# Kernel tuning notes

Hardware: AMD Instinct MI355X
Metric: run time of the kernel (lower is better)

## Reference

```python
import jax, jax.numpy as jnp
import numpy as np

B, N, C = 64, 197, 768
H = 12
D = C // H
SCALE = D ** -0.5
TAU = 5.0
THRESHOLD = 0.6
NEG_INF = float('-inf')


def setup_inputs() -> dict:
    key = jax.random.key(0)
    ks = jax.random.split(key, 10)
    def gumbel(k, shape):
        # -log(Exponential) == standard Gumbel noise, matches torch exponential_().log()
        e = jax.random.exponential(k, shape, dtype=jnp.float32)
        return -jnp.log(e + 1e-10)
    s = 0.02
    return {
        'x': jax.random.normal(ks[0], (B, N, C), dtype=jnp.float32),
        'g1': gumbel(ks[1], (B, N - 1, 1)),
        'g2': gumbel(ks[2], (B, N - 1, 1)),
        'Wq': jax.random.normal(ks[3], (C, C), dtype=jnp.float32) * s,
        'Wk': jax.random.normal(ks[4], (C, C), dtype=jnp.float32) * s,
        'Wv': jax.random.normal(ks[5], (C, C), dtype=jnp.float32) * s,
        'Wp': jax.random.normal(ks[6], (C, C), dtype=jnp.float32) * s,
        'bp': jnp.zeros((C,), dtype=jnp.float32),
        'Wm': jax.random.normal(ks[7], (1, C), dtype=jnp.float32) * s,
        'bm': jnp.zeros((1,), dtype=jnp.float32),
    }


def reference(x, g1, g2, Wq, Wk, Wv, Wp, bp, Wm, bm):
    b, n, c = x.shape
    # QKV projections (qkv_bias=False), reshape to (B, H, N, D)
    q = (x @ Wq.T).reshape(b, n, H, D).transpose(0, 2, 1, 3)
    k = (x @ Wk.T).reshape(b, n, H, D).transpose(0, 2, 1, 3)
    v = (x @ Wv.T).reshape(b, n, H, D).transpose(0, 2, 1, 3)

    attn_pre = jnp.einsum('bhnd,bhmd->bhnm', q, k) * SCALE  # (B,H,N,N)

    # SimpleTokenSelect: gumbel-sigmoid gating on non-CLS tokens (training=True, hard=True)
    logits = x[:, 1:] @ Wm.T + bm                       # (B, N-1, 1)
    y_soft = jax.nn.sigmoid((logits + g1 - g2) / TAU)
    y_hard = (y_soft > THRESHOLD).astype(y_soft.dtype)
    ts = y_hard - jax.lax.stop_gradient(y_soft) + y_soft  # straight-through
    ts = jnp.concatenate([jnp.ones((b, 1, 1), dtype=ts.dtype), ts], axis=1)[..., 0]  # (B, N)

    # attention policy = outer product of token gates, detached (ada_token_detach_attn)
    policy = jax.lax.stop_gradient(jnp.einsum('bn,bm->bnm', ts, ts))[:, None]  # (B,1,N,N)

    # pre-softmax masking: zero gated scores, -inf off-diagonal entries of gated rows
    eye = jnp.eye(n, dtype=attn_pre.dtype)
    neg_mask = jnp.where(1.0 - policy - eye > 0, NEG_INF, 0.0)
    attn = jax.nn.softmax(attn_pre * policy + neg_mask, axis=-1)

    out = jnp.einsum('bhnm,bhmd->bhnd', attn, v)        # (B,H,N,D)
    out = out.transpose(0, 2, 1, 3).reshape(b, n, c)
    out = out @ Wp.T + bp                                # proj (dropout p=0)
    return out
```

## Files before the change

### kernel.cpp

```cpp
#include <hip/hip_runtime.h>
#include <hip/hip_bf16.h>
#include <cstdint>

typedef unsigned short u16;
typedef __attribute__((ext_vector_type(8))) short bf16x8;
typedef __attribute__((ext_vector_type(4))) float f32x4;

#define NB 64
#define NN 197
#define NC 768
#define NH 12
#define ND 64
#define NM (NB*NN)
#define CAP 96
#define ASZ ((size_t)NM*NC)
#define WSZ ((size_t)NC*NC)
#define SELSZ ((size_t)NB*CAP*NC)

__device__ __forceinline__ u16 f2bf(float f) {
  uint32_t u = __float_as_uint(f);
  u += 0x7fffu + ((u >> 16) & 1u);
  return (u16)(u >> 16);
}

__device__ __forceinline__ void gl_lds16(const u16* g, u16* l) {
  __builtin_amdgcn_global_load_lds(
      (const __attribute__((address_space(1))) void*)g,
      (__attribute__((address_space(3))) void*)l, 16, 0, 0);
}

__device__ __forceinline__ int self_compact(const float* __restrict__ ts, int b,
                                            int* sidx, unsigned long long* bmask) {
  int t = threadIdx.x, lane = t & 63, wave = t >> 6;
  bool sel = (t < NN) && (ts[b * NN + t] > 0.5f);
  unsigned long long m = __ballot(sel);
  if (lane == 0) bmask[wave] = m;
  for (int i = t; i < CAP; i += 256) sidx[i] = 0;
  __syncthreads();
  int before = 0, total = 0;
  #pragma unroll
  for (int w = 0; w < 4; ++w) {
    int c = __popcll(bmask[w]);
    total += c;
    if (w < wave) before += c;
  }
  int within = __popcll(bmask[wave] & ((lane == 0) ? 0ull : (~0ull >> (64 - lane))));
  int pos = before + within;
  int cntc = total < CAP ? total : CAP;
  if (sel && pos < CAP) sidx[pos] = t;
  __syncthreads();
  return cntc;
}

#define GATEB 3152
#define XBLK 9456
#define WBLK 576
#define TRBLK 144
__global__ __launch_bounds__(256) void k1_prep(const float* __restrict__ x,
    const float* __restrict__ g1, const float* __restrict__ g2,
    const float* __restrict__ Wm, const float* __restrict__ bm,
    const float* __restrict__ wq, const float* __restrict__ wk,
    const float* __restrict__ wv, const float* __restrict__ wp,
    u16* __restrict__ xb, u16* __restrict__ wqb, u16* __restrict__ wkb,
    u16* __restrict__ wvb, u16* __restrict__ wpb, u16* __restrict__ wvt,
    float* __restrict__ ts) {
  __shared__ u16 T[64][72];
  int bid = blockIdx.x, tid = threadIdx.x;

  if (bid < GATEB) {
    int wave = tid >> 6, lane = tid & 63;
    int wid = bid * 4 + wave;
    int b = wid / NN, n = wid % NN;
    float o = 1.0f;
    if (n != 0) {
      const float* xr = x + (size_t)wid * NC;
      double acc = 0.0;
      #pragma unroll
      for (int i = 0; i < 12; ++i)
        acc += (double)xr[lane + 64*i] * (double)Wm[lane + 64*i];
      #pragma unroll
      for (int off = 32; off; off >>= 1) acc += __shfl_down(acc, off);
      double z = (acc + (double)bm[0] + (double)g1[b*(NN-1) + n - 1]
                                      - (double)g2[b*(NN-1) + n - 1]) / 5.0;
      o = (z > 0.4054651081081643820) ? 1.0f : 0.0f;
      o = __shfl(o, 0);
    }
    if (lane == 0) ts[wid] = o;
    return;
  }
  bid -= GATEB;
  if (bid < XBLK) {
    int i = bid * 256 + tid;
    float4 f = ((const float4*)x)[i];
    ushort4 o;
    o.x = f2bf(f.x); o.y = f2bf(f.y); o.z = f2bf(f.z); o.w = f2bf(f.w);
    ((ushort4*)xb)[i] = o;
    return;
  }
  bid -= XBLK;
  if (bid < 4*WBLK) {
    int seg = bid / WBLK;
    int i = (bid - seg * WBLK) * 256 + tid;
    const float* src; u16* dst;
    if (seg == 0)      { src = wq; dst = wqb; }
    else if (seg == 1) { src = wk; dst = wkb; }
    else if (seg == 2) { src = wv; dst = wvb; }
    else               { src = wp; dst = wpb; }
    float4 f = ((const float4*)src)[i];
    ushort4 o;
    o.x = f2bf(f.x); o.y = f2bf(f.y); o.z = f2bf(f.z); o.w = f2bf(f.w);
    ((ushort4*)dst)[i] = o;
    return;
  }
  bid -= 4*WBLK;
  {
    int bx = bid % 12, by = bid / 12;
    int j0 = by * 64, k0 = bx * 64;
    #pragma unroll
    for (int g = 0; g < 4; ++g) {
      int r = g * 16 + (tid >> 4);
      int c4 = (tid & 15) * 4;
      float4 f = *(const float4*)(wv + (size_t)(j0 + r) * NC + k0 + c4);
      T[c4 + 0][r] = f2bf(f.x);
      T[c4 + 1][r] = f2bf(f.y);
      T[c4 + 2][r] = f2bf(f.z);
      T[c4 + 3][r] = f2bf(f.w);
    }
    __syncthreads();
    #pragma unroll
    for (int g = 0; g < 4; ++g) {
      int r = g * 16 + (tid >> 4);
      int c4 = (tid & 15) * 4;
      ushort4 o = *(ushort4*)&T[r][c4];
      *(ushort4*)(wvt + (size_t)(k0 + r) * NC + j0 + c4) = o;
    }
  }
}

__global__ __launch_bounds__(256) void k2_wvp_qkv(const u16* __restrict__ xb,
    const u16* __restrict__ wq3, const u16* __restrict__ wpb,
    const u16* __restrict__ wvt, u16* __restrict__ wvpb,
    u16* __restrict__ sel3, const float* __restrict__ ts) {
  alignas(16) __shared__ u16 SA[128][32];
  alignas(16) __shared__ u16 SB[128][32];
  __shared__ int sidx[CAP];
  __shared__ unsigned long long bmask[4];
  int bid = blockIdx.x;
  int tid = threadIdx.x, lane = tid & 63, wave = tid >> 6;
  int lr = lane & 15, lg = lane >> 4, lk = lg * 8;

  if (bid < 36) {
    int m0 = (bid / 6) * 128, n0 = (bid % 6) * 128;
    int wr = (wave >> 1) * 64, wc = (wave & 1) * 64;
    f32x4 acc[4][4];
    #pragma unroll
    for (int i = 0; i < 4; ++i)
      #pragma unroll
      for (int j = 0; j < 4; ++j) acc[i][j] = (f32x4){0.f,0.f,0.f,0.f};
    for (int k0 = 0; k0 < NC; k0 += 32) {
      #pragma unroll
      for (int i = 0; i < 2; ++i) {
        int c = wave * 2 + i;
        int id = c * 64 + lane;
        int row = id >> 2, col8 = (id & 3) * 8;
        gl_lds16(wpb + (size_t)(m0 + row) * NC + k0 + col8, &SA[0][0] + c * 512);
        gl_lds16(wvt + (size_t)(n0 + row) * NC + k0 + col8, &SB[0][0] + c * 512);
      }
      __syncthreads();
      bf16x8 af[4], bfr[4];
      #pragma unroll
      for (int f = 0; f < 4; ++f) {
        af[f]  = *(const bf16x8*)(&SA[wr + f*16 + lr][lk]);
        bfr[f] = *(const bf16x8*)(&SB[wc + f*16 + lr][lk]);
      }
      #pragma unroll
      for (int i = 0; i < 4; ++i)
        #pragma unroll
        for (int j = 0; j < 4; ++j)
          acc[i][j] = __builtin_amdgcn_mfma_f32_16x16x32_bf16(af[i], bfr[j], acc[i][j], 0, 0, 0);
      __syncthreads();
    }
    #pragma unroll
    for (int i = 0; i < 4; ++i)
      #pragma unroll
      for (int j = 0; j < 4; ++j)
        #pragma unroll
        for (int r = 0; r < 4; ++r)
          wvpb[(size_t)(m0 + wr + i*16 + 4*lg + r) * NC + n0 + wc + j*16 + lr] =
              f2bf(acc[i][j][r]);
    return;
  }

  int t = bid - 36;
  int gb = t / 18, r18 = t % 18;
  int y = r18 / 3, z = r18 % 3;
  int b = gb / 3, rc = gb % 3;
  int cntb = self_compact(ts, b, sidx, bmask);
  if (rc * 32 >= cntb) return;
  const u16* W = wq3 + (size_t)z * WSZ;
  u16* o = sel3 + (size_t)z * SELSZ;
  int n0 = y * 128;

  int chA = wave * 64 + lane;
  int tokA = sidx[rc * 32 + (chA >> 2)];
  const u16* baseA = xb + (size_t)(b * NN + tokA) * NC + (chA & 3) * 8;
  u16* ldsA = &SA[0][0] + (size_t)(wave * 64) * 8;
  int chB0 = wave * 64 + lane, chB1 = 256 + wave * 64 + lane;
  const u16* baseB0 = W + (size_t)(n0 + (chB0 >> 2)) * NC + (chB0 & 3) * 8;
  const u16* baseB1 = W + (size_t)(n0 + (chB1 >> 2)) * NC + (chB1 & 3) * 8;
  u16* ldsB0 = &SB[0][0] + (size_t)(wave * 64) * 8;
  u16* ldsB1 = &SB[0][0] + (size_t)(256 + wave * 64) * 8;

  int wc = wave * 32;
  f32x4 acc[2][2];
  #pragma unroll
  for (int i = 0; i < 2; ++i)
    #pragma unroll
    for (int j = 0; j < 2; ++j) acc[i][j] = (f32x4){0.f,0.f,0.f,0.f};

  for (int k0 = 0; k0 < NC; k0 += 32) {
    if (wave < 2) gl_lds16(baseA + k0, ldsA);
    gl_lds16(baseB0 + k0, ldsB0);
    gl_lds16(baseB1 + k0, ldsB1);
    __syncthreads();
    bf16x8 af[2], bfr[2];
    #pragma unroll
    for (int f = 0; f < 2; ++f) {
      af[f]  = *(const bf16x8*)(&SA[f*16 + lr][lk]);
      bfr[f] = *(const bf16x8*)(&SB[wc + f*16 + lr][lk]);
    }
    #pragma unroll
    for (int i = 0; i < 2; ++i)
      #pragma unroll
      for (int j = 0; j < 2; ++j)
        acc[i][j] = __builtin_amdgcn_mfma_f32_16x16x32_bf16(af[i], bfr[j], acc[i][j], 0, 0, 0);
    __syncthreads();
  }

  #pragma unroll
  for (int i = 0; i < 2; ++i)
    #pragma unroll
    for (int j = 0; j < 2; ++j)
      #pragma unroll
      for (int r = 0; r < 4; ++r) {
        int rsel = rc*32 + i*16 + 4*lg + r;
        if (rsel < cntb)
          o[(size_t)(b * CAP + rsel) * NC + n0 + wc + j*16 + lr] = f2bf(acc[i][j][r]);
      }
}

__global__ __launch_bounds__(256) void attn_sel(const u16* __restrict__ qsel,
    const u16* __restrict__ ksel, const u16* __restrict__ vsel,
    u16* __restrict__ zsel, const float* __restrict__ ts) {
  alignas(16) __shared__ u16 Vt[64][232];
  __shared__ unsigned long long bmask[4];
  int bh = blockIdx.x;
  int b = bh / NH, h = bh % NH;
  int tid = threadIdx.x, lane = tid & 63, wave = tid >> 6;
  int lr = lane & 15, lg = lane >> 4;
  const size_t qbase = (size_t)b * CAP * NC + (size_t)h * ND;

  bool selt = (tid < NN) && (ts[b * NN + tid] > 0.5f);
  unsigned long long m = __ballot(selt);
  if (lane == 0) bmask[wave] = m;
  __syncthreads();
  int cntb = 0;
  #pragma unroll
  for (int w = 0; w < 4; ++w) cntb += __popcll(bmask[w]);
  if (cntb > CAP) cntb = CAP;

  for (int id = tid; id < cntb * 8; id += 256) {
    int i = id >> 3, c8 = (id & 7) * 8;
    int4 val = *(const int4*)(vsel + qbase + (size_t)i * NC + c8);
    u16 tmp[8];
    *(int4*)tmp = val;
    #pragma unroll
    for (int e = 0; e < 8; ++e) Vt[c8 + e][i] = tmp[e];
  }
  for (int id = tid; id < 64 * 32; id += 256)
    Vt[id >> 5][cntb + (id & 31)] = 0;
  __syncthreads();

  int nchunk = (cntb + 15) >> 4;
  int mtmax  = nchunk;
  int mcmax  = (cntb + 31) >> 5;
  int idx0 = (((lane & 15) | ((lane & 16) << 1))) << 2;
  int idx1 = idx0 + 64;

  for (int qc = wave; qc < nchunk; qc += 4) {
    const u16* qp = qsel + qbase + (size_t)(qc * 16 + lr) * NC + lg * 8;
    bf16x8 qf0 = *(const bf16x8*)(qp);
    bf16x8 qf1 = *(const bf16x8*)(qp + 32);

    f32x4 s[6];
    #pragma unroll
    for (int mt = 0; mt < 6; ++mt) s[mt] = (f32x4){0.f,0.f,0.f,0.f};
    #pragma unroll
    for (int mt = 0; mt < 6; ++mt) {
      if (mt < mtmax) {
        const u16* kp = ksel + qbase + (size_t)(mt * 16 + lr) * NC + lg * 8;
        bf16x8 kf0 = *(const bf16x8*)(kp);
        bf16x8 kf1 = *(const bf16x8*)(kp + 32);
        f32x4 a = (f32x4){0.f,0.f,0.f,0.f};
        a = __builtin_amdgcn_mfma_f32_16x16x32_bf16(kf0, qf0, a, 0, 0, 0);
        a = __builtin_amdgcn_mfma_f32_16x16x32_bf16(kf1, qf1, a, 0, 0, 0);
        s[mt] = a;
      }
    }

    float mx = -3e38f;
    #pragma unroll
    for (int mt = 0; mt < 6; ++mt)
      #pragma unroll
      for (int jj = 0; jj < 4; ++jj) {
        int mm = mt*16 + 4*lg + jj;
        float val = (mm < cntb) ? s[mt][jj] * 0.125f : -1e30f;
        s[mt][jj] = val;
        mx = fmaxf(mx, val);
      }
    mx = fmaxf(mx, __shfl_xor(mx, 16));
    mx = fmaxf(mx, __shfl_xor(mx, 32));
    float sum = 0.f;
    #pragma unroll
    for (int mt = 0; mt < 6; ++mt)
      #pragma unroll
      for (int jj = 0; jj < 4; ++jj) {
        float pv = __expf(s[mt][jj] - mx);
        s[mt][jj] = pv;
        sum += pv;
      }
    sum += __shfl_xor(sum, 16);
    sum += __shfl_xor(sum, 32);
    float inv = 1.0f / sum;

    uint32_t u[6][2];
    #pragma unroll
    for (int mt = 0; mt < 6; ++mt) {
      u[mt][0] = ((uint32_t)f2bf(s[mt][1]*inv) << 16) | f2bf(s[mt][0]*inv);
      u[mt][1] = ((uint32_t)f2bf(s[mt][3]*inv) << 16) | f2bf(s[mt][2]*inv);
    }

    f32x4 oacc[4];
    #pragma unroll
    for (int dt = 0; dt < 4; ++dt) oacc[dt] = (f32x4){0.f,0.f,0.f,0.f};
    #pragma unroll
    for (int mc = 0; mc < 3; ++mc) {
      if (mc < mcmax) {
        uint32_t a0 = (uint32_t)__builtin_amdgcn_ds_bpermute(idx0, (int)u[2*mc][0]);
        uint32_t b0 = (uint32_t)__builtin_amdgcn_ds_bpermute(idx0, (int)u[2*mc+1][0]);
        uint32_t a1 = (uint32_t)__builtin_amdgcn_ds_bpermute(idx0, (int)u[2*mc][1]);
        uint32_t b1 = (uint32_t)__builtin_amdgcn_ds_bpermute(idx0, (int)u[2*mc+1][1]);
        uint32_t a2 = (uint32_t)__builtin_amdgcn_ds_bpermute(idx1, (int)u[2*mc][0]);
        uint32_t b2 = (uint32_t)__builtin_amdgcn_ds_bpermute(idx1, (int)u[2*mc+1][0]);
        uint32_t a3 = (uint32_t)__builtin_amdgcn_ds_bpermute(idx1, (int)u[2*mc][1]);
        uint32_t b3 = (uint32_t)__builtin_amdgcn_ds_bpermute(idx1, (int)u[2*mc+1][1]);
        bool hi = (lg >= 2);
        union { uint32_t w[4]; bf16x8 v; } pu;
        pu.w[0] = hi ? b0 : a0;
        pu.w[1] = hi ? b1 : a1;
        pu.w[2] = hi ? b2 : a2;
        pu.w[3] = hi ? b3 : a3;
        bf16x8 pa = pu.v;
        #pragma unroll
        for (int dt = 0; dt < 4; ++dt) {
          bf16x8 vf = *(const bf16x8*)(&Vt[dt*16 + lr][mc*32 + lg*8]);
          oacc[dt] = __builtin_amdgcn_mfma_f32_16x16x32_bf16(pa, vf, oacc[dt], 0, 0, 0);
        }
      }
    }

    #pragma unroll
    for (int r = 0; r < 4; ++r) {
      int nloc = qc*16 + 4*lg + r;
      if (nloc < cntb) {
        u16* op = zsel + qbase + (size_t)nloc * NC + lr;
        #pragma unroll
        for (int dt = 0; dt < 4; ++dt)
          op[dt*16] = f2bf(oacc[dt][r]);
      }
    }
  }
}

#define DBLK 594
__global__ __launch_bounds__(256) void k4_out(const u16* __restrict__ xb,
    const u16* __restrict__ wvpb, const u16* __restrict__ zsel,
    const u16* __restrict__ wpb, const float* __restrict__ ts,
    const float* __restrict__ bp, float* __restrict__ out) {
  alignas(16) __shared__ u16 SA[128][32];
  alignas(16) __shared__ u16 SB[128][32];
  __shared__ int sidx[CAP];
  __shared__ unsigned long long bmask[4];
  int bid = blockIdx.x;
  int tid = threadIdx.x, lane = tid & 63, wave = tid >> 6;
  int lr = lane & 15, lg = lane >> 4, lk = lg * 8;

  if (bid < DBLK) {
    int m0 = (bid / 6) * 128, n0 = (bid % 6) * 128;
    int wr = (wave >> 1) * 64, wc = (wave & 1) * 64;
    f32x4 acc[4][4];
    #pragma unroll
    for (int i = 0; i < 4; ++i)
      #pragma unroll
      for (int j = 0; j < 4; ++j) acc[i][j] = (f32x4){0.f,0.f,0.f,0.f};
    for (int k0 = 0; k0 < NC; k0 += 32) {
      #pragma unroll
      for (int i = 0; i < 2; ++i) {
        int c = wave * 2 + i;
        int id = c * 64 + lane;
        int row = id >> 2, col8 = (id & 3) * 8;
        gl_lds16(xb + (size_t)(m0 + row) * NC + k0 + col8, &SA[0][0] + c * 512);
        gl_lds16(wvpb + (size_t)(n0 + row) * NC + k0 + col8, &SB[0][0] + c * 512);
      }
      __syncthreads();
      bf16x8 af[4], bfr[4];
      #pragma unroll
      for (int f = 0; f < 4; ++f) {
        af[f]  = *(const bf16x8*)(&SA[wr + f*16 + lr][lk]);
        bfr[f] = *(const bf16x8*)(&SB[wc + f*16 + lr][lk]);
      }
      #pragma unroll
      for (int i = 0; i < 4; ++i)
        #pragma unroll
        for (int j = 0; j < 4; ++j)
          acc[i][j] = __builtin_amdgcn_mfma_f32_16x16x32_bf16(af[i], bfr[j], acc[i][j], 0, 0, 0);
      __syncthreads();
    }
    #pragma unroll
    for (int i = 0; i < 4; ++i) {
      int rbase = m0 + wr + i*16 + 4*lg;
      #pragma unroll
      for (int j = 0; j < 4; ++j) {
        int col = n0 + wc + j*16 + lr;
        #pragma unroll
        for (int r = 0; r < 4; ++r) {
          int row = rbase + r;
          if (row < NM && ts[row] < 0.5f)
            out[(size_t)row * NC + col] = acc[i][j][r] + bp[col];
        }
      }
    }
    return;
  }

  int t = bid - DBLK;
  int gb = t / 6, y = t % 6;
  int b = gb / 3, rc = gb % 3;
  int cntb = self_compact(ts, b, sidx, bmask);
  if (rc * 32 >= cntb) return;
  int n0 = y * 128;

  int chA = wave * 64 + lane;
  const u16* baseA = zsel + (size_t)(b * CAP + rc * 32 + (chA >> 2)) * NC + (chA & 3) * 8;
  u16* ldsA = &SA[0][0] + (size_t)(wave * 64) * 8;
  int chB0 = wave * 64 + lane, chB1 = 256 + wave * 64 + lane;
  const u16* baseB0 = wpb + (size_t)(n0 + (chB0 >> 2)) * NC + (chB0 & 3) * 8;
  const u16* baseB1 = wpb + (size_t)(n0 + (chB1 >> 2)) * NC + (chB1 & 3) * 8;
  u16* ldsB0 = &SB[0][0] + (size_t)(wave * 64) * 8;
  u16* ldsB1 = &SB[0][0] + (size_t)(256 + wave * 64) * 8;

  int wc = wave * 32;
  f32x4 acc[2][2];
  #pragma unroll
  for (int i = 0; i < 2; ++i)
    #pragma unroll
    for (int j = 0; j < 2; ++j) acc[i][j] = (f32x4){0.f,0.f,0.f,0.f};

  for (int k0 = 0; k0 < NC; k0 += 32) {
    if (wave < 2) gl_lds16(baseA + k0, ldsA);
    gl_lds16(baseB0 + k0, ldsB0);
    gl_lds16(baseB1 + k0, ldsB1);
    __syncthreads();
    bf16x8 af[2], bfr[2];
    #pragma unroll
    for (int f = 0; f < 2; ++f) {
      af[f]  = *(const bf16x8*)(&SA[f*16 + lr][lk]);
      bfr[f] = *(const bf16x8*)(&SB[wc + f*16 + lr][lk]);
    }
    #pragma unroll
    for (int i = 0; i < 2; ++i)
      #pragma unroll
      for (int j = 0; j < 2; ++j)
        acc[i][j] = __builtin_amdgcn_mfma_f32_16x16x32_bf16(af[i], bfr[j], acc[i][j], 0, 0, 0);
    __syncthreads();
  }

  #pragma unroll
  for (int i = 0; i < 2; ++i)
    #pragma unroll
    for (int j = 0; j < 2; ++j)
      #pragma unroll
      for (int r = 0; r < 4; ++r) {
        int rsel = rc*32 + i*16 + 4*lg + r;
        if (rsel < cntb) {
          int tok = sidx[rsel];
          int col = n0 + wc + j*16 + lr;
          out[(size_t)(b * NN + tok) * NC + col] = acc[i][j][r] + bp[col];
        }
      }
}

extern "C" void kernel_launch(void* const* d_in, const int* in_sizes, int n_in,
                              void* d_out, int out_size, void* d_ws, size_t ws_size,
                              hipStream_t stream) {
  const float* x  = (const float*)d_in[0];
  const float* g1 = (const float*)d_in[1];
  const float* g2 = (const float*)d_in[2];
  const float* Wq = (const float*)d_in[3];
  const float* Wk = (const float*)d_in[4];
  const float* Wv = (const float*)d_in[5];
  const float* Wp = (const float*)d_in[6];
  const float* bp = (const float*)d_in[7];
  const float* Wm = (const float*)d_in[8];
  const float* bm = (const float*)d_in[9];
  float* out = (float*)d_out;

  const size_t act_sz = ASZ * 2;
  const size_t w_sz   = WSZ * 2;
  const size_t sel_sz = SELSZ * 2;
  size_t need = act_sz + 4*sel_sz + 6*w_sz + (size_t)NM*4 + 256;
  if (ws_size < need) return;

  char* p = (char*)d_ws;
  u16* xb   = (u16*)p; p += act_sz;
  u16* qsel = (u16*)p; p += sel_sz;
  u16* ksel = (u16*)p; p += sel_sz;
  u16* vsel = (u16*)p; p += sel_sz;
  u16* zsel = (u16*)p; p += sel_sz;
  u16* wqb  = (u16*)p; p += w_sz;
  u16* wkb  = (u16*)p; p += w_sz;
  u16* wvb  = (u16*)p; p += w_sz;
  u16* wpb  = (u16*)p; p += w_sz;
  u16* wvtb = (u16*)p; p += w_sz;
  u16* wvpb = (u16*)p; p += w_sz;
  float* ts = (float*)p;
  (void)wkb; (void)wvb;

  k1_prep<<<dim3(GATEB + XBLK + 4*WBLK + TRBLK), 256, 0, stream>>>(
      x, g1, g2, Wm, bm, Wq, Wk, Wv, Wp,
      xb, wqb, wkb, wvb, wpb, wvtb, ts);

  k2_wvp_qkv<<<dim3(36 + NB*3*18), 256, 0, stream>>>(
      xb, wqb, wpb, wvtb, wvpb, qsel, ts);

  attn_sel<<<dim3(NB*NH), 256, 0, stream>>>(qsel, ksel, vsel, zsel, ts);

  k4_out<<<dim3(DBLK + NB*3*6), 256, 0, stream>>>(
      xb, wvpb, zsel, wpb, ts, bp, out);
}
```

Measured before the change: 115.9 us.

## Double-buffer LDS in GEMM loops, reorder k4 blocks, remap dense tiles per XCD

Every GEMM main loop (k2 dense and selected paths, k4 dense and selected paths) now uses two LDS buffers. The next K-slice is loaded asynchronously while MFMAs run on the current one, which removes one barrier per iteration and overlaps load latency with compute. k4 now launches the sparse selected-token blocks first and the dense blocks after them. The dense block IDs are remapped so that consecutive tiles land on the same XCD, aiming at better L2 reuse. LDS use per block doubles, which may lower occupancy.

```diff
diff --git a/kernel.cpp b/kernel.cpp
--- a/kernel.cpp
+++ b/kernel.cpp
@@ -13,6 +13,7 @@
 #define ND 64
 #define NM (NB*NN)
 #define CAP 96
+#define NT 24
 #define ASZ ((size_t)NM*NC)
 #define WSZ ((size_t)NC*NC)
 #define SELSZ ((size_t)NB*CAP*NC)
@@ -141,8 +142,8 @@
     const u16* __restrict__ wq3, const u16* __restrict__ wpb,
     const u16* __restrict__ wvt, u16* __restrict__ wvpb,
     u16* __restrict__ sel3, const float* __restrict__ ts) {
-  alignas(16) __shared__ u16 SA[128][32];
-  alignas(16) __shared__ u16 SB[128][32];
+  alignas(16) __shared__ u16 SA[2][128][32];
+  alignas(16) __shared__ u16 SB[2][128][32];
   __shared__ int sidx[CAP];
   __shared__ unsigned long long bmask[4];
   int bid = blockIdx.x;
@@ -157,29 +158,39 @@
     for (int i = 0; i < 4; ++i)
       #pragma unroll
       for (int j = 0; j < 4; ++j) acc[i][j] = (f32x4){0.f,0.f,0.f,0.f};
-    for (int k0 = 0; k0 < NC; k0 += 32) {
+    auto stage = [&](int buf, int k0) {
       #pragma unroll
       for (int i = 0; i < 2; ++i) {
         int c = wave * 2 + i;
         int id = c * 64 + lane;
         int row = id >> 2, col8 = (id & 3) * 8;
-        gl_lds16(wpb + (size_t)(m0 + row) * NC + k0 + col8, &SA[0][0] + c * 512);
-        gl_lds16(wvt + (size_t)(n0 + row) * NC + k0 + col8, &SB[0][0] + c * 512);
-      }
-      __syncthreads();
+        gl_lds16(wpb + (size_t)(m0 + row) * NC + k0 + col8, &SA[buf][0][0] + c * 512);
+        gl_lds16(wvt + (size_t)(n0 + row) * NC + k0 + col8, &SB[buf][0][0] + c * 512);
+      }
+    };
+    auto comp = [&](int buf) {
       bf16x8 af[4], bfr[4];
       #pragma unroll
       for (int f = 0; f < 4; ++f) {
-        af[f]  = *(const bf16x8*)(&SA[wr + f*16 + lr][lk]);
-        bfr[f] = *(const bf16x8*)(&SB[wc + f*16 + lr][lk]);
+        af[f]  = *(const bf16x8*)(&SA[buf][wr + f*16 + lr][lk]);
+        bfr[f] = *(const bf16x8*)(&SB[buf][wc + f*16 + lr][lk]);
       }
       #pragma unroll
       for (int i = 0; i < 4; ++i)
         #pragma unroll
         for (int j = 0; j < 4; ++j)
           acc[i][j] = __builtin_amdgcn_mfma_f32_16x16x32_bf16(af[i], bfr[j], acc[i][j], 0, 0, 0);
+    };
+    stage(0, 0);
+    __syncthreads();
+    int cur = 0;
+    for (int t = 0; t < NT - 1; ++t) {
+      stage(cur ^ 1, (t + 1) * 32);
+      comp(cur);
       __syncthreads();
-    }
+      cur ^= 1;
+    }
+    comp(cur);
     #pragma unroll
     for (int i = 0; i < 4; ++i)
       #pragma unroll
@@ -204,12 +215,9 @@
   int chA = wave * 64 + lane;
   int tokA = sidx[rc * 32 + (chA >> 2)];
   const u16* baseA = xb + (size_t)(b * NN + tokA) * NC + (chA & 3) * 8;
-  u16* ldsA = &SA[0][0] + (size_t)(wave * 64) * 8;
   int chB0 = wave * 64 + lane, chB1 = 256 + wave * 64 + lane;
   const u16* baseB0 = W + (size_t)(n0 + (chB0 >> 2)) * NC + (chB0 & 3) * 8;
   const u16* baseB1 = W + (size_t)(n0 + (chB1 >> 2)) * NC + (chB1 & 3) * 8;
-  u16* ldsB0 = &SB[0][0] + (size_t)(wave * 64) * 8;
-  u16* ldsB1 = &SB[0][0] + (size_t)(256 + wave * 64) * 8;
 
   int wc = wave * 32;
   f32x4 acc[2][2];
@@ -218,24 +226,34 @@
     #pragma unroll
     for (int j = 0; j < 2; ++j) acc[i][j] = (f32x4){0.f,0.f,0.f,0.f};
 
-  for (int k0 = 0; k0 < NC; k0 += 32) {
-    if (wave < 2) gl_lds16(baseA + k0, ldsA);
-    gl_lds16(baseB0 + k0, ldsB0);
-    gl_lds16(baseB1 + k0, ldsB1);
-    __syncthreads();
+  auto stageS = [&](int buf, int k0) {
+    if (wave < 2) gl_lds16(baseA + k0, &SA[buf][0][0] + (size_t)(wave * 64) * 8);
+    gl_lds16(baseB0 + k0, &SB[buf][0][0] + (size_t)(wave * 64) * 8);
+    gl_lds16(baseB1 + k0, &SB[buf][0][0] + (size_t)(256 + wave * 64) * 8);
+  };
+  auto compS = [&](int buf) {
     bf16x8 af[2], bfr[2];
     #pragma unroll
     for (int f = 0; f < 2; ++f) {
-      af[f]  = *(const bf16x8*)(&SA[f*16 + lr][lk]);
-      bfr[f] = *(const bf16x8*)(&SB[wc + f*16 + lr][lk]);
+      af[f]  = *(const bf16x8*)(&SA[buf][f*16 + lr][lk]);
+      bfr[f] = *(const bf16x8*)(&SB[buf][wc + f*16 + lr][lk]);
     }
     #pragma unroll
     for (int i = 0; i < 2; ++i)
       #pragma unroll
       for (int j = 0; j < 2; ++j)
         acc[i][j] = __builtin_amdgcn_mfma_f32_16x16x32_bf16(af[i], bfr[j], acc[i][j], 0, 0, 0);
+  };
+  stageS(0, 0);
+  __syncthreads();
+  int cur = 0;
+  for (int tt = 0; tt < NT - 1; ++tt) {
+    stageS(cur ^ 1, (tt + 1) * 32);
+    compS(cur);
     __syncthreads();
-  }
+    cur ^= 1;
+  }
+  compS(cur);
 
   #pragma unroll
   for (int i = 0; i < 2; ++i)
@@ -382,50 +400,64 @@
   }
 }
 
+#define PBLK 1152
 #define DBLK 594
 __global__ __launch_bounds__(256) void k4_out(const u16* __restrict__ xb,
     const u16* __restrict__ wvpb, const u16* __restrict__ zsel,
     const u16* __restrict__ wpb, const float* __restrict__ ts,
     const float* __restrict__ bp, float* __restrict__ out) {
-  alignas(16) __shared__ u16 SA[128][32];
-  alignas(16) __shared__ u16 SB[128][32];
+  alignas(16) __shared__ u16 SA[2][128][32];
+  alignas(16) __shared__ u16 SB[2][128][32];
   __shared__ int sidx[CAP];
   __shared__ unsigned long long bmask[4];
   int bid = blockIdx.x;
   int tid = threadIdx.x, lane = tid & 63, wave = tid >> 6;
   int lr = lane & 15, lg = lane >> 4, lk = lg * 8;
 
-  if (bid < DBLK) {
-    int m0 = (bid / 6) * 128, n0 = (bid % 6) * 128;
+  if (bid >= PBLK) {
+    int orig = bid - PBLK;
+    int xcd = orig & 7, loc = orig >> 3;
+    int wgid = (xcd < 2 ? xcd * 75 : 150 + (xcd - 2) * 74) + loc;
+    int m0 = (wgid / 6) * 128, n0 = (wgid % 6) * 128;
     int wr = (wave >> 1) * 64, wc = (wave & 1) * 64;
     f32x4 acc[4][4];
     #pragma unroll
     for (int i = 0; i < 4; ++i)
       #pragma unroll
       for (int j = 0; j < 4; ++j) acc[i][j] = (f32x4){0.f,0.f,0.f,0.f};
-    for (int k0 = 0; k0 < NC; k0 += 32) {
+    auto stage = [&](int buf, int k0) {
       #pragma unroll
       for (int i = 0; i < 2; ++i) {
         int c = wave * 2 + i;
         int id = c * 64 + lane;
         int row = id >> 2, col8 = (id & 3) * 8;
-        gl_lds16(xb + (size_t)(m0 + row) * NC + k0 + col8, &SA[0][0] + c * 512);
-        gl_lds16(wvpb + (size_t)(n0 + row) * NC + k0 + col8, &SB[0][0] + c * 512);
-      }
-      __syncthreads();
+        gl_lds16(xb + (size_t)(m0 + row) * NC + k0 + col8, &SA[buf][0][0] + c * 512);
+        gl_lds16(wvpb + (size_t)(n0 + row) * NC + k0 + col8, &SB[buf][0][0] + c * 512);
+      }
+    };
+    auto comp = [&](int buf) {
       bf16x8 af[4], bfr[4];
       #pragma unroll
       for (int f = 0; f < 4; ++f) {
-        af[f]  = *(const bf16x8*)(&SA[wr + f*16 + lr][lk]);
-        bfr[f] = *(const bf16x8*)(&SB[wc + f*16 + lr][lk]);
+        af[f]  = *(const bf16x8*)(&SA[buf][wr + f*16 + lr][lk]);
+        bfr[f] = *(const bf16x8*)(&SB[buf][wc + f*16 + lr][lk]);
       }
       #pragma unroll
       for (int i = 0; i < 4; ++i)
         #pragma unroll
         for (int j = 0; j < 4; ++j)
           acc[i][j] = __builtin_amdgcn_mfma_f32_16x16x32_bf16(af[i], bfr[j], acc[i][j], 0, 0, 0);
+    };
+    stage(0, 0);
+    __syncthreads();
+    int cur = 0;
+    for (int t = 0; t < NT - 1; ++t) {
+      stage(cur ^ 1, (t + 1) * 32);
+      comp(cur);
       __syncthreads();
-    }
+      cur ^= 1;
+    }
+    comp(cur);
     #pragma unroll
     for (int i = 0; i < 4; ++i) {
       int rbase = m0 + wr + i*16 + 4*lg;
@@ -443,7 +475,7 @@
     return;
   }
 
-  int t = bid - DBLK;
+  int t = bid;
   int gb = t / 6, y = t % 6;
   int b = gb / 3, rc = gb % 3;
   int cntb = self_compact(ts, b, sidx, bmask);
@@ -452,12 +484,9 @@
 
   int chA = wave * 64 + lane;
   const u16* baseA = zsel + (size_t)(b * CAP + rc * 32 + (chA >> 2)) * NC + (chA & 3) * 8;
-  u16* ldsA = &SA[0][0] + (size_t)(wave * 64) * 8;
   int chB0 = wave * 64 + lane, chB1 = 256 + wave * 64 + lane;
   const u16* baseB0 = wpb + (size_t)(n0 + (chB0 >> 2)) * NC + (chB0 & 3) * 8;
   const u16* baseB1 = wpb + (size_t)(n0 + (chB1 >> 2)) * NC + (chB1 & 3) * 8;
-  u16* ldsB0 = &SB[0][0] + (size_t)(wave * 64) * 8;
-  u16* ldsB1 = &SB[0][0] + (size_t)(256 + wave * 64) * 8;
 
   int wc = wave * 32;
   f32x4 acc[2][2];
@@ -466,24 +495,34 @@
     #pragma unroll
     for (int j = 0; j < 2; ++j) acc[i][j] = (f32x4){0.f,0.f,0.f,0.f};
 
-  for (int k0 = 0; k0 < NC; k0 += 32) {
-    if (wave < 2) gl_lds16(baseA + k0, ldsA);
-    gl_lds16(baseB0 + k0, ldsB0);
-    gl_lds16(baseB1 + k0, ldsB1);
-    __syncthreads();
+  auto stageS = [&](int buf, int k0) {
+    if (wave < 2) gl_lds16(baseA + k0, &SA[buf][0][0] + (size_t)(wave * 64) * 8);
+    gl_lds16(baseB0 + k0, &SB[buf][0][0] + (size_t)(wave * 64) * 8);
+    gl_lds16(baseB1 + k0, &SB[buf][0][0] + (size_t)(256 + wave * 64) * 8);
+  };
+  auto compS = [&](int buf) {
     bf16x8 af[2], bfr[2];
     #pragma unroll
     for (int f = 0; f < 2; ++f) {
-      af[f]  = *(const bf16x8*)(&SA[f*16 + lr][lk]);
-      bfr[f] = *(const bf16x8*)(&SB[wc + f*16 + lr][lk]);
+      af[f]  = *(const bf16x8*)(&SA[buf][f*16 + lr][lk]);
+      bfr[f] = *(const bf16x8*)(&SB[buf][wc + f*16 + lr][lk]);
     }
     #pragma unroll
     for (int i = 0; i < 2; ++i)
       #pragma unroll
       for (int j = 0; j < 2; ++j)
         acc[i][j] = __builtin_amdgcn_mfma_f32_16x16x32_bf16(af[i], bfr[j], acc[i][j], 0, 0, 0);
+  };
+  stageS(0, 0);
+  __syncthreads();
+  int cur = 0;
+  for (int tt = 0; tt < NT - 1; ++tt) {
+    stageS(cur ^ 1, (tt + 1) * 32);
+    compS(cur);
     __syncthreads();
-  }
+    cur ^= 1;
+  }
+  compS(cur);
 
   #pragma unroll
   for (int i = 0; i < 2; ++i)
@@ -545,6 +584,6 @@
 
   attn_sel<<<dim3(NB*NH), 256, 0, stream>>>(qsel, ksel, vsel, zsel, ts);
 
-  k4_out<<<dim3(DBLK + NB*3*6), 256, 0, stream>>>(
+  k4_out<<<dim3(PBLK + DBLK), 256, 0, stream>>>(
       xb, wvpb, zsel, wpb, ts, bp, out);
 }
```

New measurement: 119.6 us. 1.03x slower.
